# Optimization experiments

Measured on AMD Instinct MI355X. Metric: run time of the kernel, lower is better.

## Reference

```python
import jax, jax.numpy as jnp
import numpy as np

N_INPUTS = 64
N_OUTPUTS = 64
N_OPS = 8  # ('none','linear','power_two','power_three','exp','ln','reciprocal','sin')
BATCH = 65536
TEMP = 1.0


def setup_inputs() -> dict:
    key = jax.random.key(0)
    k1, k2, k3 = jax.random.split(key, 3)
    # shift inputs into (0.5, 1.5) so ln / reciprocal are well-behaved
    x = jax.random.uniform(k1, (BATCH, N_INPUTS), dtype=jnp.float32) + 0.5
    alphas = 0.001 * jax.random.normal(k2, (N_INPUTS, N_OUTPUTS, N_OPS), dtype=jnp.float32)
    coeffs = jax.random.normal(k3, (N_INPUTS, N_OUTPUTS, N_OPS), dtype=jnp.float32)
    return {"x": x, "alphas": alphas, "coeffs": coeffs}


def _primitives(x):
    # x: [B, I] -> [B, I, N_OPS], one channel per primitive op
    return jnp.stack(
        [
            jnp.zeros_like(x),   # none
            x,                   # linear
            x * x,               # power_two
            x * x * x,           # power_three
            jnp.exp(x),          # exp
            jnp.log(x),          # ln
            1.0 / x,             # reciprocal
            jnp.sin(x),          # sin
        ],
        axis=-1,
    )


def reference(x, alphas, coeffs):
    # softmax gating over primitives (non-discrete, non-gumbel branch)
    gates = jax.nn.softmax(alphas / TEMP, axis=-1)        # [I, J, K]
    prims = _primitives(x)                                # [B, I, K]
    # operation_outputs[b,i,j] = sum_k gates[i,j,k] * coeffs[i,j,k] * prims[b,i,k]
    # layer_output[b,j] = sum_i operation_outputs[b,i,j]
    w = gates * coeffs                                    # [I, J, K]
    out = jnp.einsum("bik,ijk->bj", prims, w)            # [B, J]
    return out
```

## Files before the change

kernel.cpp:

```cpp
#include <hip/hip_runtime.h>
#include <hip/hip_bf16.h>
#include <stdint.h>


typedef __bf16 bf16x8 __attribute__((ext_vector_type(8)));
typedef float f32x4 __attribute__((ext_vector_type(4)));

#define LOG2E   1.4426950408889634f
#define LN2     0.6931471805599453f
#define INV2PI  0.15915494309189535f

__global__ __launch_bounds__(1024, 4) void darts_fused(const float* __restrict__ x,
                                                       const float* __restrict__ alphas,
                                                       const float* __restrict__ coeffs,
                                                       float* __restrict__ out) {
    __shared__ __bf16 wlds[32768];

    const int tid  = threadIdx.x;
    const int lane = tid & 63;
    const int wv   = tid >> 6;
    const int m    = lane & 15;
    const int q    = lane >> 4;

    const int row = blockIdx.x * 256 + wv * 16 + m;
    const float* xp = x + row * 64 + q * 16;
    f32x4 xr0 = *(const f32x4*)(xp + 0);
    f32x4 xr1 = *(const f32x4*)(xp + 4);
    f32x4 xr2 = *(const f32x4*)(xp + 8);
    f32x4 xr3 = *(const f32x4*)(xp + 12);

#pragma unroll
    for (int u = 0; u < 4; ++u) {
        const int g = u * 1024 + tid;
        const int i = g >> 6;
        const int n = g & 63;
        const float* a  = alphas + g * 8;
        const float* cf = coeffs + g * 8;

        float e[8], s = 0.f;
#pragma unroll
        for (int k = 0; k < 8; ++k) {
            e[k] = __builtin_amdgcn_exp2f(a[k] * LOG2E);
            s += e[k];
        }
        const float inv = __builtin_amdgcn_rcpf(s);

        bf16x8 w;
#pragma unroll
        for (int k = 0; k < 8; ++k) w[k] = (__bf16)(e[k] * inv * cf[k]);

        const int qq = i >> 4, cc = i & 15, t = n >> 4, nl = n & 15;
        *(bf16x8*)(wlds + ((cc * 4 + t) * 64 + qq * 16 + nl) * 8) = w;
    }
    __syncthreads();

    float xa[16];
#pragma unroll
    for (int c = 0; c < 4; ++c) { xa[c] = xr0[c]; xa[4+c] = xr1[c]; xa[8+c] = xr2[c]; xa[12+c] = xr3[c]; }

    f32x4 acc0 = {0.f, 0.f, 0.f, 0.f};
    f32x4 acc1 = {0.f, 0.f, 0.f, 0.f};
    f32x4 acc2 = {0.f, 0.f, 0.f, 0.f};
    f32x4 acc3 = {0.f, 0.f, 0.f, 0.f};

#pragma unroll
    for (int c = 0; c < 16; ++c) {
        const float xv = xa[c];
        const float x2 = xv * xv;
        bf16x8 a;
        a[0] = (__bf16)0.0f;
        a[1] = (__bf16)xv;
        a[2] = (__bf16)x2;
        a[3] = (__bf16)(x2 * xv);
        a[4] = (__bf16)__builtin_amdgcn_exp2f(xv * LOG2E);
        a[5] = (__bf16)(__builtin_amdgcn_logf(xv) * LN2);
        a[6] = (__bf16)__builtin_amdgcn_rcpf(xv);
        a[7] = (__bf16)__builtin_amdgcn_sinf(xv * INV2PI);
        const __bf16* bb = wlds + c * 2048 + lane * 8;
        bf16x8 b0 = *(const bf16x8*)(bb);
        bf16x8 b1 = *(const bf16x8*)(bb + 512);
        bf16x8 b2 = *(const bf16x8*)(bb + 1024);
        bf16x8 b3 = *(const bf16x8*)(bb + 1536);
        acc0 = __builtin_amdgcn_mfma_f32_16x16x32_bf16(a, b0, acc0, 0, 0, 0);
        acc1 = __builtin_amdgcn_mfma_f32_16x16x32_bf16(a, b1, acc1, 0, 0, 0);
        acc2 = __builtin_amdgcn_mfma_f32_16x16x32_bf16(a, b2, acc2, 0, 0, 0);
        acc3 = __builtin_amdgcn_mfma_f32_16x16x32_bf16(a, b3, acc3, 0, 0, 0);
    }

    float* orow = out + (blockIdx.x * 256 + wv * 16 + q * 4) * 64 + m;
#pragma unroll
    for (int r = 0; r < 4; ++r) {
        orow[r * 64 + 0]  = acc0[r];
        orow[r * 64 + 16] = acc1[r];
        orow[r * 64 + 32] = acc2[r];
        orow[r * 64 + 48] = acc3[r];
    }
}

extern "C" void kernel_launch(void* const* d_in, const int* in_sizes, int n_in,
                              void* d_out, int out_size, void* d_ws, size_t ws_size,
                              hipStream_t stream) {
    const float* x      = (const float*)d_in[0];
    const float* alphas = (const float*)d_in[1];
    const float* coeffs = (const float*)d_in[2];
    float* out = (float*)d_out;
    (void)d_ws; (void)ws_size;

    darts_fused<<<256, 1024, 0, stream>>>(x, alphas, coeffs, out);
}
```

Before: 76.88 us.

## Give each wave two row tiles to reuse LDS weight fragments across MFMAs

Halves the block to 512 threads and has each wave compute 32 rows (two 16-row MFMA tiles), so every B fragment read from LDS feeds two MFMAs instead of one. The weight-build loop is also remapped so each thread writes its LDS slot linearly and gathers from permuted alphas/coeffs addresses, replacing a scattered LDS write with scattered global reads. The aim is to cut LDS read traffic per MFMA. In exchange it raises register pressure, doubles the per-thread softmax prologue work, and lowers the thread count per CU.

Measured after the change: 78.33 us. No clear change (+1.9%).

```diff
diff --git a/kernel.cpp b/kernel.cpp
--- a/kernel.cpp
+++ b/kernel.cpp
@@ -10,10 +10,24 @@
 #define LN2     0.6931471805599453f
 #define INV2PI  0.15915494309189535f
 
-__global__ __launch_bounds__(1024, 4) void darts_fused(const float* __restrict__ x,
-                                                       const float* __restrict__ alphas,
-                                                       const float* __restrict__ coeffs,
-                                                       float* __restrict__ out) {
+__device__ __forceinline__ bf16x8 prim_frag(float xv) {
+    const float x2 = xv * xv;
+    bf16x8 a;
+    a[0] = (__bf16)0.0f;
+    a[1] = (__bf16)xv;
+    a[2] = (__bf16)x2;
+    a[3] = (__bf16)(x2 * xv);
+    a[4] = (__bf16)__builtin_amdgcn_exp2f(xv * LOG2E);
+    a[5] = (__bf16)(__builtin_amdgcn_logf(xv) * LN2);
+    a[6] = (__bf16)__builtin_amdgcn_rcpf(xv);
+    a[7] = (__bf16)__builtin_amdgcn_sinf(xv * INV2PI);
+    return a;
+}
+
+__global__ __launch_bounds__(512, 2) void darts_fused(const float* __restrict__ x,
+                                                      const float* __restrict__ alphas,
+                                                      const float* __restrict__ coeffs,
+                                                      float* __restrict__ out) {
     __shared__ __bf16 wlds[32768];
 
     const int tid  = threadIdx.x;
@@ -22,20 +36,28 @@
     const int m    = lane & 15;
     const int q    = lane >> 4;
 
-    const int row = blockIdx.x * 256 + wv * 16 + m;
-    const float* xp = x + row * 64 + q * 16;
-    f32x4 xr0 = *(const f32x4*)(xp + 0);
-    f32x4 xr1 = *(const f32x4*)(xp + 4);
-    f32x4 xr2 = *(const f32x4*)(xp + 8);
-    f32x4 xr3 = *(const f32x4*)(xp + 12);
+    const int row0 = blockIdx.x * 256 + wv * 32 + m;
+    const float* xp0 = x + row0 * 64 + q * 16;
+    f32x4 x00 = *(const f32x4*)(xp0 + 0);
+    f32x4 x01 = *(const f32x4*)(xp0 + 4);
+    f32x4 x02 = *(const f32x4*)(xp0 + 8);
+    f32x4 x03 = *(const f32x4*)(xp0 + 12);
+    const float* xp1 = xp0 + 16 * 64;
+    f32x4 x10 = *(const f32x4*)(xp1 + 0);
+    f32x4 x11 = *(const f32x4*)(xp1 + 4);
+    f32x4 x12 = *(const f32x4*)(xp1 + 8);
+    f32x4 x13 = *(const f32x4*)(xp1 + 12);
 
 #pragma unroll
-    for (int u = 0; u < 4; ++u) {
-        const int g = u * 1024 + tid;
-        const int i = g >> 6;
-        const int n = g & 63;
-        const float* a  = alphas + g * 8;
-        const float* cf = coeffs + g * 8;
+    for (int u = 0; u < 8; ++u) {
+        const int gp = u * 512 + tid;
+        const int cc = gp >> 8;
+        const int t  = (gp >> 6) & 3;
+        const int qq = (gp >> 4) & 3;
+        const int nl = gp & 15;
+        const int src = ((qq * 16 + cc) * 64 + t * 16 + nl) * 8;
+        const float* a  = alphas + src;
+        const float* cf = coeffs + src;
 
         float e[8], s = 0.f;
 #pragma unroll
@@ -49,51 +71,53 @@
 #pragma unroll
         for (int k = 0; k < 8; ++k) w[k] = (__bf16)(e[k] * inv * cf[k]);
 
-        const int qq = i >> 4, cc = i & 15, t = n >> 4, nl = n & 15;
-        *(bf16x8*)(wlds + ((cc * 4 + t) * 64 + qq * 16 + nl) * 8) = w;
+        *(bf16x8*)(wlds + gp * 8) = w;
     }
     __syncthreads();
 
-    float xa[16];
+    float xa0[16], xa1[16];
 #pragma unroll
-    for (int c = 0; c < 4; ++c) { xa[c] = xr0[c]; xa[4+c] = xr1[c]; xa[8+c] = xr2[c]; xa[12+c] = xr3[c]; }
+    for (int c = 0; c < 4; ++c) {
+        xa0[c] = x00[c]; xa0[4 + c] = x01[c]; xa0[8 + c] = x02[c]; xa0[12 + c] = x03[c];
+        xa1[c] = x10[c]; xa1[4 + c] = x11[c]; xa1[8 + c] = x12[c]; xa1[12 + c] = x13[c];
+    }
 
-    f32x4 acc0 = {0.f, 0.f, 0.f, 0.f};
-    f32x4 acc1 = {0.f, 0.f, 0.f, 0.f};
-    f32x4 acc2 = {0.f, 0.f, 0.f, 0.f};
-    f32x4 acc3 = {0.f, 0.f, 0.f, 0.f};
+    f32x4 acc00 = {0.f, 0.f, 0.f, 0.f}, acc01 = {0.f, 0.f, 0.f, 0.f};
+    f32x4 acc02 = {0.f, 0.f, 0.f, 0.f}, acc03 = {0.f, 0.f, 0.f, 0.f};
+    f32x4 acc10 = {0.f, 0.f, 0.f, 0.f}, acc11 = {0.f, 0.f, 0.f, 0.f};
+    f32x4 acc12 = {0.f, 0.f, 0.f, 0.f}, acc13 = {0.f, 0.f, 0.f, 0.f};
 
 #pragma unroll
     for (int c = 0; c < 16; ++c) {
-        const float xv = xa[c];
-        const float x2 = xv * xv;
-        bf16x8 a;
-        a[0] = (__bf16)0.0f;
-        a[1] = (__bf16)xv;
-        a[2] = (__bf16)x2;
-        a[3] = (__bf16)(x2 * xv);
-        a[4] = (__bf16)__builtin_amdgcn_exp2f(xv * LOG2E);
-        a[5] = (__bf16)(__builtin_amdgcn_logf(xv) * LN2);
-        a[6] = (__bf16)__builtin_amdgcn_rcpf(xv);
-        a[7] = (__bf16)__builtin_amdgcn_sinf(xv * INV2PI);
+        bf16x8 a0 = prim_frag(xa0[c]);
+        bf16x8 a1 = prim_frag(xa1[c]);
         const __bf16* bb = wlds + c * 2048 + lane * 8;
         bf16x8 b0 = *(const bf16x8*)(bb);
         bf16x8 b1 = *(const bf16x8*)(bb + 512);
         bf16x8 b2 = *(const bf16x8*)(bb + 1024);
         bf16x8 b3 = *(const bf16x8*)(bb + 1536);
-        acc0 = __builtin_amdgcn_mfma_f32_16x16x32_bf16(a, b0, acc0, 0, 0, 0);
-        acc1 = __builtin_amdgcn_mfma_f32_16x16x32_bf16(a, b1, acc1, 0, 0, 0);
-        acc2 = __builtin_amdgcn_mfma_f32_16x16x32_bf16(a, b2, acc2, 0, 0, 0);
-        acc3 = __builtin_amdgcn_mfma_f32_16x16x32_bf16(a, b3, acc3, 0, 0, 0);
+        acc00 = __builtin_amdgcn_mfma_f32_16x16x32_bf16(a0, b0, acc00, 0, 0, 0);
+        acc10 = __builtin_amdgcn_mfma_f32_16x16x32_bf16(a1, b0, acc10, 0, 0, 0);
+        acc01 = __builtin_amdgcn_mfma_f32_16x16x32_bf16(a0, b1, acc01, 0, 0, 0);
+        acc11 = __builtin_amdgcn_mfma_f32_16x16x32_bf16(a1, b1, acc11, 0, 0, 0);
+        acc02 = __builtin_amdgcn_mfma_f32_16x16x32_bf16(a0, b2, acc02, 0, 0, 0);
+        acc12 = __builtin_amdgcn_mfma_f32_16x16x32_bf16(a1, b2, acc12, 0, 0, 0);
+        acc03 = __builtin_amdgcn_mfma_f32_16x16x32_bf16(a0, b3, acc03, 0, 0, 0);
+        acc13 = __builtin_amdgcn_mfma_f32_16x16x32_bf16(a1, b3, acc13, 0, 0, 0);
     }
 
-    float* orow = out + (blockIdx.x * 256 + wv * 16 + q * 4) * 64 + m;
+    float* o0 = out + (blockIdx.x * 256 + wv * 32 + q * 4) * 64 + m;
+    float* o1 = o0 + 16 * 64;
 #pragma unroll
     for (int r = 0; r < 4; ++r) {
-        orow[r * 64 + 0]  = acc0[r];
-        orow[r * 64 + 16] = acc1[r];
-        orow[r * 64 + 32] = acc2[r];
-        orow[r * 64 + 48] = acc3[r];
+        o0[r * 64 + 0]  = acc00[r];
+        o0[r * 64 + 16] = acc01[r];
+        o0[r * 64 + 32] = acc02[r];
+        o0[r * 64 + 48] = acc03[r];
+        o1[r * 64 + 0]  = acc10[r];
+        o1[r * 64 + 16] = acc11[r];
+        o1[r * 64 + 32] = acc12[r];
+        o1[r * 64 + 48] = acc13[r];
     }
 }
 
@@ -106,5 +130,5 @@
     float* out = (float*)d_out;
     (void)d_ws; (void)ws_size;
 
-    darts_fused<<<256, 1024, 0, stream>>>(x, alphas, coeffs, out);
+    darts_fused<<<256, 512, 0, stream>>>(x, alphas, coeffs, out);
 }
```
